# Optimization experiments

Measured on AMD Instinct MI355X. Metric: run time of the kernel, lower is better.

Reference implementation:

```python
import jax, jax.numpy as jnp
import numpy as np

D_MODEL = 1024
D_STATE = 16
D_CONV = 4
EXPAND = 1
D_INNER = EXPAND * D_MODEL  # must equal D_MODEL for original dt_proj shapes to work
BATCH = 2
SEQ = 2048


def silu(x):
    return x * jax.nn.sigmoid(x)


def setup_inputs() -> dict:
    key = jax.random.key(0)
    ks = jax.random.split(key, 8)
    s = 0.02
    return {
        "x": jax.random.normal(ks[0], (BATCH, SEQ, D_MODEL), dtype=jnp.float32),
        "W_in": jax.random.normal(ks[1], (2 * D_INNER, D_MODEL), dtype=jnp.float32) * s,
        "conv_w": jax.random.normal(ks[2], (D_INNER, D_CONV), dtype=jnp.float32) * s,
        "conv_b": jnp.zeros((D_INNER,), dtype=jnp.float32),
        "W_dt": jax.random.normal(ks[3], (D_INNER, D_INNER), dtype=jnp.float32) * s,
        "b_dt": jnp.zeros((D_INNER,), dtype=jnp.float32),
        "A_log": jnp.zeros((D_INNER, D_STATE), dtype=jnp.float32),  # torch: log(ones)=0
        "Bp": jax.random.normal(ks[4], (D_INNER, D_STATE), dtype=jnp.float32),
        "Cp": jax.random.normal(ks[5], (D_INNER, D_STATE), dtype=jnp.float32),
        "Dp": jnp.ones((D_INNER,), dtype=jnp.float32),
        "W_out": jax.random.normal(ks[6], (D_MODEL, D_INNER), dtype=jnp.float32) * s,
    }


def reference(x, W_in, conv_w, conv_b, W_dt, b_dt, A_log, Bp, Cp, Dp, W_out):
    B, L, _ = x.shape
    # in_proj then split into ssm branch and gating residual
    xr = x @ W_in.T                               # (B, L, 2*D_INNER)
    x_proj, res = jnp.split(xr, 2, axis=-1)       # each (B, L, D_INNER)

    # causal depthwise conv1d (kernel D_CONV), == torch conv1d(padding=K-1)[..., :L]
    xp = jnp.pad(x_proj, ((0, 0), (D_CONV - 1, 0), (0, 0)))
    xc = conv_b + sum(conv_w[:, k] * xp[:, k:k + L, :] for k in range(D_CONV))
    xc = silu(xc)                                 # (B, L, D_INNER)

    # selective SSM scan
    delta = jax.nn.softplus(xc @ W_dt.T + b_dt)   # (B, L, D_INNER)
    A = -jnp.exp(A_log)                           # (D_INNER, D_STATE)
    dA = jnp.exp(delta[..., None] * A)            # (B, L, D_INNER, D_STATE)
    dBx = delta[..., None] * Bp * xc[..., None]   # (B, L, D_INNER, D_STATE)

    def step(h, inp):
        dA_t, dBx_t = inp                         # (B, D_INNER, D_STATE)
        h = dA_t * h + dBx_t
        y = jnp.einsum('bdn,dn->bd', h, Cp)
        return h, y

    h0 = jnp.zeros((B, D_INNER, D_STATE), dtype=x.dtype)
    _, ys = jax.lax.scan(step, h0, (dA.transpose(1, 0, 2, 3), dBx.transpose(1, 0, 2, 3)))
    x_ssm = ys.transpose(1, 0, 2) + xc * Dp       # (B, L, D_INNER)

    return (x_ssm * silu(res)) @ W_out.T          # (B, L, D_MODEL)
```

## Files before the change

### kernel.cpp

```cpp
#include <hip/hip_runtime.h>

typedef unsigned short u16;
typedef __bf16 bf16;
typedef bf16 bf16x8 __attribute__((ext_vector_type(8)));
typedef float f32x16 __attribute__((ext_vector_type(16)));

#define SEQ     2048
#define BATCH   2
#define DM      1024
#define DI      1024
#define NROW    (BATCH*SEQ)
#define NSTATE  16
#define NCHUNK  64
#define CLEN    32
#define BK      64

static_assert(SEQ == NCHUNK * CLEN, "chunking must cover SEQ");

__device__ __forceinline__ u16 f2bf(float f) {
  unsigned u = __builtin_bit_cast(unsigned, f);
  u += 0x7FFFu + ((u >> 16) & 1u);
  return (u16)(u >> 16);
}
__device__ __forceinline__ float bf2f(u16 u) {
  return __builtin_bit_cast(float, (unsigned)u << 16);
}
__device__ __forceinline__ float sigm(float x) { return 1.f / (1.f + __expf(-x)); }

__global__ __launch_bounds__(256) void k_cvt_all(
    const float* __restrict__ x, const float* __restrict__ Win,
    const float* __restrict__ Wdt, const float* __restrict__ Wout,
    u16* __restrict__ xbf, u16* __restrict__ winbf,
    u16* __restrict__ wdtbf, u16* __restrict__ woutbf)
{
  long i = (long)blockIdx.x * 256 + threadIdx.x;
  const float* src; u16* dst; long off;
  if (i < 1048576)            { src = x;    dst = xbf;    off = i; }
  else if (i < 1572864)       { src = Win;  dst = winbf;  off = i - 1048576; }
  else if (i < 1835008)       { src = Wdt;  dst = wdtbf;  off = i - 1572864; }
  else                        { src = Wout; dst = woutbf; off = i - 1835008; }
  float4 v = reinterpret_cast<const float4*>(src)[off];
  ushort4 o;
  o.x = f2bf(v.x); o.y = f2bf(v.y); o.z = f2bf(v.z); o.w = f2bf(v.w);
  reinterpret_cast<ushort4*>(dst)[off] = o;
}


__device__ __forceinline__ void gload16(const u16* g, u16* l) {
  __builtin_amdgcn_global_load_lds((const __attribute__((address_space(1))) void*)g,
                                   (__attribute__((address_space(3))) void*)l,
                                   16, 0, 0);
}

template<int EPI, int BM, int BN, int GX, int MINW>
__global__ __launch_bounds__(256, MINW) void k_gemm(
    const u16* __restrict__ A, const u16* __restrict__ B,
    float* __restrict__ outf, u16* __restrict__ outb, u16* __restrict__ outb2,
    const float* __restrict__ bias,
    const float* __restrict__ A_log, const float* __restrict__ Bp,
    float* __restrict__ hfin, float* __restrict__ sumdt,
    int M, int N, int K)
{
  constexpr int MI_ = BM / 64;
  constexpr int NI_ = BN / 64;
  __shared__ __align__(16) u16 sA[2 * BM * BK];
  __shared__ __align__(16) u16 sB[2 * BN * BK];
  const int t = threadIdx.x;
  const int wave = t >> 6, lane = t & 63;
  const int la = lane & 31, hi = lane >> 5;
  const int wr = wave >> 1, wc = wave & 1;

  const int nwg = gridDim.x;
  const int bid = blockIdx.x;
  const int wg  = (bid & 7) * (nwg >> 3) + (bid >> 3);
  const long bm = (long)(wg / GX) * BM;
  const long bn = (long)(wg % GX) * BN;

  f32x16 acc[MI_][NI_] = {};

  const int srow = t >> 3;
  const int gslot8 = (((t & 7) ^ (srow & 7)) * 8);
  const u16* gA0 = A + (bm + srow) * (long)K + gslot8;
  const u16* gB0 = B + (bn + srow) * (long)K + gslot8;

  auto STAGE = [&](int buf, int k0) {
    #pragma unroll
    for (int i = 0; i < BM / 32; ++i)
      gload16(gA0 + (long)i * 32 * K + k0,
              &sA[buf * (BM * BK) + i * 2048 + wave * 512]);
    #pragma unroll
    for (int i = 0; i < BN / 32; ++i)
      gload16(gB0 + (long)i * 32 * K + k0,
              &sB[buf * (BN * BK) + i * 2048 + wave * 512]);
  };

  const int xr = la & 7;
  STAGE(0, 0);
  __syncthreads();
  int cur = 0;
  for (int k0 = 0; k0 < K; k0 += BK) {
    if (k0 + BK < K) STAGE(cur ^ 1, k0 + BK);
    const u16* pa = &sA[cur * (BM * BK)];
    const u16* pb = &sB[cur * (BN * BK)];
    bf16x8 af[4][MI_], bfr[4][NI_];
    #pragma unroll
    for (int ks = 0; ks < 4; ++ks) {
      const int co = ((ks * 2 + hi) ^ xr) * 8;
      #pragma unroll
      for (int mi = 0; mi < MI_; ++mi)
        af[ks][mi] = *reinterpret_cast<const bf16x8*>(
            pa + (wr * (BM / 2) + mi * 32 + la) * BK + co);
      #pragma unroll
      for (int ni = 0; ni < NI_; ++ni)
        bfr[ks][ni] = *reinterpret_cast<const bf16x8*>(
            pb + (wc * (BN / 2) + ni * 32 + la) * BK + co);
    }
    __builtin_amdgcn_s_setprio(1);
    #pragma unroll
    for (int ks = 0; ks < 4; ++ks)
      #pragma unroll
      for (int mi = 0; mi < MI_; ++mi)
        #pragma unroll
        for (int ni = 0; ni < NI_; ++ni)
          acc[mi][ni] = __builtin_amdgcn_mfma_f32_32x32x16_bf16(
              af[ks][mi], bfr[ks][ni], acc[mi][ni], 0, 0, 0);
    __builtin_amdgcn_s_setprio(0);
    __syncthreads();
    cur ^= 1;
  }

  float* sDelta = (float*)sA;

  #pragma unroll
  for (int mi = 0; mi < MI_; ++mi) {
    const long rowb = bm + wr * (BM / 2) + mi * 32 + 4 * hi;
    #pragma unroll
    for (int ni = 0; ni < NI_; ++ni) {
      const long col = bn + wc * (BN / 2) + ni * 32 + la;
      #pragma unroll
      for (int q = 0; q < 4; ++q)
        #pragma unroll
        for (int j = 0; j < 4; ++j) {
          const float v = acc[mi][ni][q * 4 + j];
          const long r = rowb + q * 8 + j;
          if (EPI == 0) {
            outf[r * N + col] = v;
          } else if (EPI == 1) {
            if (bn < DI) outb[r * DI + col] = f2bf(v);
            else         outb2[r * DI + (col - DI)] = f2bf(v * sigm(v));
          } else if (EPI == 3) {
            float z = v + bias[col];
            float sp = fmaxf(z, 0.f) + log1pf(__expf(-fabsf(z)));
            outb[r * N + col] = f2bf(sp);
            sDelta[(int)(r - bm) * 64 + (int)(col - bn)] = sp;
          }
        }
    }
  }

  if (EPI == 3) {
    __syncthreads();
    const int pair = t >> 1, half = t & 1;
    const int clocal = pair >> 6;
    const int dl = pair & 63;
    const int d = (int)bn + dl;
    const int b = (int)(bm >> 11);
    const int cglob = (int)((bm & 2047) >> 5) + clocal;
    const long grow0 = bm + clocal * 32;
    float Aa[8], Bb[8], h[8];
    #pragma unroll
    for (int n = 0; n < 8; ++n) {
      Aa[n] = -__expf(A_log[d * NSTATE + half * 8 + n]);
      Bb[n] = Bp[d * NSTATE + half * 8 + n];
      h[n] = 0.f;
    }
    float sdt = 0.f;
    for (int i = 0; i < CLEN; ++i) {
      float dt = sDelta[(clocal * 32 + i) * 64 + dl];
      float xv = bf2f(A[(grow0 + i) * (long)K + d]);
      sdt += dt;
      float dx = dt * xv;
      #pragma unroll
      for (int n = 0; n < 8; ++n) {
        float da = __expf(dt * Aa[n]);
        h[n] = fmaf(da, h[n], dx * Bb[n]);
      }
    }
    const long hb = ((long)(b * NCHUNK + cglob) * NSTATE + half * 8) * DI + d;
    #pragma unroll
    for (int n = 0; n < 8; ++n) hfin[hb + (long)n * DI] = h[n];
    if (half == 0) sumdt[(long)(b * NCHUNK + cglob) * DI + d] = sdt;
  }
}

__global__ __launch_bounds__(256) void k_conv(
    const u16* __restrict__ xproj, const float* __restrict__ convw,
    const float* __restrict__ convb, u16* __restrict__ xcbf)
{
  const int idx = blockIdx.x * 256 + threadIdx.x;
  const int d0 = (idx & 127) * 8;
  const int m  = idx >> 7;
  const int l  = m & (SEQ - 1);
  float acc[8];
  #pragma unroll
  for (int di = 0; di < 8; ++di) acc[di] = convb[d0 + di];
  #pragma unroll
  for (int k = 0; k < 4; ++k) {
    if (l + k - 3 >= 0) {
      ushort4 v2 = *reinterpret_cast<const ushort4*>(&xproj[(long)(m + k - 3) * DI + d0]);
      ushort4 v3 = *reinterpret_cast<const ushort4*>(&xproj[(long)(m + k - 3) * DI + d0 + 4]);
      const u16 vv[8] = {v2.x, v2.y, v2.z, v2.w, v3.x, v3.y, v3.z, v3.w};
      #pragma unroll
      for (int di = 0; di < 8; ++di)
        acc[di] = fmaf(convw[(d0 + di) * 4 + k], bf2f(vv[di]), acc[di]);
    }
  }
  ushort4 o0, o1;
  u16 ov[8];
  #pragma unroll
  for (int di = 0; di < 8; ++di) {
    float s = acc[di] * sigm(acc[di]);
    ov[di] = f2bf(s);
  }
  o0 = {ov[0], ov[1], ov[2], ov[3]}; o1 = {ov[4], ov[5], ov[6], ov[7]};
  *reinterpret_cast<ushort4*>(&xcbf[(long)m * DI + d0]) = o0;
  *reinterpret_cast<ushort4*>(&xcbf[(long)m * DI + d0 + 4]) = o1;
}

__global__ __launch_bounds__(256) void k_combine(
    const float* __restrict__ hfin, const float* __restrict__ sumdt_buf,
    const float* __restrict__ A_log, float* __restrict__ hstart)
{
  const int idx = blockIdx.x * 256 + threadIdx.x;
  const int d = idx & (DI - 1);
  const int n = (idx >> 10) & (NSTATE - 1);
  const int b = idx >> 14;
  const float Aa = -__expf(A_log[d * NSTATE + n]);
  float h = 0.f;
  for (int c = 0; c < NCHUNK; ++c) {
    const long sb = ((long)(b * NCHUNK + c) * NSTATE + n) * DI + d;
    hstart[sb] = h;
    float sdt = sumdt_buf[(long)(b * NCHUNK + c) * DI + d];
    h = fmaf(__expf(Aa * sdt), h, hfin[sb]);
  }
}

__global__ __launch_bounds__(256) void k_scanB(
    const u16* __restrict__ delta, const u16* __restrict__ xc,
    const float* __restrict__ A_log, const float* __restrict__ Bp,
    const float* __restrict__ Cp, const float* __restrict__ Dp,
    const u16* __restrict__ sres, const float* __restrict__ hstart,
    u16* __restrict__ gated)
{
  const int tid = threadIdx.x, blk = blockIdx.x;
  const int d = (blk & 3) * 256 + tid;
  const int c = (blk >> 2) & (NCHUNK - 1);
  const int b = blk >> 8;
  float Aa[NSTATE], Bb[NSTATE], Cc[NSTATE], h[NSTATE];
  #pragma unroll
  for (int n = 0; n < NSTATE; ++n) {
    Aa[n] = -__expf(A_log[d * NSTATE + n]);
    Bb[n] = Bp[d * NSTATE + n];
    Cc[n] = Cp[d * NSTATE + n];
  }
  const float Dd = Dp[d];
  const long sb = ((long)(b * NCHUNK + c) * NSTATE) * DI + d;
  #pragma unroll
  for (int n = 0; n < NSTATE; ++n) h[n] = hstart[sb + (long)n * DI];
  const long base = ((long)(b * SEQ + c * CLEN)) * DI + d;
  for (int i = 0; i < CLEN; ++i) {
    float dt = bf2f(delta[base + (long)i * DI]);
    float x  = bf2f(xc[base + (long)i * DI]);
    float dx = dt * x;
    float y = 0.f;
    #pragma unroll
    for (int n = 0; n < NSTATE; ++n) {
      float da = __expf(dt * Aa[n]);
      h[n] = fmaf(da, h[n], dx * Bb[n]);
      y = fmaf(h[n], Cc[n], y);
    }
    float xs = fmaf(x, Dd, y);
    float g = xs * bf2f(sres[base + (long)i * DI]);
    gated[base + (long)i * DI] = f2bf(g);
  }
}

extern "C" void kernel_launch(void* const* d_in, const int* in_sizes, int n_in,
                              void* d_out, int out_size, void* d_ws, size_t ws_size,
                              hipStream_t stream)
{
  const float* x      = (const float*)d_in[0];
  const float* W_in   = (const float*)d_in[1];
  const float* conv_w = (const float*)d_in[2];
  const float* conv_b = (const float*)d_in[3];
  const float* W_dt   = (const float*)d_in[4];
  const float* b_dt   = (const float*)d_in[5];
  const float* A_log  = (const float*)d_in[6];
  const float* Bp     = (const float*)d_in[7];
  const float* Cp     = (const float*)d_in[8];
  const float* Dp     = (const float*)d_in[9];
  const float* W_out  = (const float*)d_in[10];
  float* out = (float*)d_out;

  const long MD = (long)NROW * DI;

  char* ws = (char*)d_ws;
  u16*   xproj_bf = (u16*)ws;               ws += MD * 2;
  u16*   silu_bf  = (u16*)ws;               ws += MD * 2;
  u16*   delta_bf = (u16*)ws;               ws += MD * 2;
  u16*   xc_bf    = (u16*)ws;               ws += MD * 2;
  u16*   xbf      = (u16*)ws;               ws += MD * 2;
  u16*   Win_bf   = (u16*)ws;               ws += (long)2 * DI * DM * 2;
  u16*   Wdt_bf   = (u16*)ws;               ws += (long)DI * DI * 2;
  u16*   Wout_bf  = (u16*)ws;               ws += (long)DM * DI * 2;
  float* hfin     = (float*)ws;             ws += (long)BATCH * NCHUNK * NSTATE * DI * 4;
  float* sumdt    = (float*)ws;             ws += (long)BATCH * NCHUNK * DI * 4;
  float* hstart   = (float*)ws;             ws += (long)BATCH * NCHUNK * NSTATE * DI * 4;

  u16* gated = xbf;

  k_cvt_all<<<dim3(8192), dim3(256), 0, stream>>>(
      x, W_in, W_dt, W_out, xbf, Win_bf, Wdt_bf, Wout_bf);

  k_gemm<1, 128, 128, 16, 2><<<dim3(512), dim3(256), 0, stream>>>(
      xbf, Win_bf, nullptr, xproj_bf, silu_bf, nullptr,
      nullptr, nullptr, nullptr, nullptr, NROW, 2 * DI, DM);

  k_conv<<<dim3((unsigned)(MD / 8 / 256)), dim3(256), 0, stream>>>(
      xproj_bf, conv_w, conv_b, xc_bf);

  k_gemm<3, 64, 64, 16, 2><<<dim3(1024), dim3(256), 0, stream>>>(
      xc_bf, Wdt_bf, nullptr, delta_bf, nullptr, b_dt,
      A_log, Bp, hfin, sumdt, NROW, DI, DI);

  k_combine<<<dim3(BATCH * NSTATE * DI / 256), dim3(256), 0, stream>>>(
      hfin, sumdt, A_log, hstart);
  k_scanB<<<dim3(BATCH * NCHUNK * (DI / 256)), dim3(256), 0, stream>>>(
      delta_bf, xc_bf, A_log, Bp, Cp, Dp, silu_bf, hstart, gated);

  k_gemm<0, 64, 64, 16, 4><<<dim3(1024), dim3(256), 0, stream>>>(
      gated, Wout_bf, out, nullptr, nullptr, nullptr,
      nullptr, nullptr, nullptr, nullptr, NROW, DM, DI);
}
```

Baseline: 165.9 us.

## Unify GEMMs on 128x128 tiles with 16x16x32 MFMA and rebalance scan epilogue

Every GEMM now uses one 128x128 tile shape computed with 16x16x32 bf16 MFMAs instead of 32x32x16. The delta and out-projection GEMMs move from 1024 blocks of 64x64 to 256 blocks of 128x128. The aim is more operand reuse per LDS load and fewer redundant global reads. The fused chunk-scan epilogue is reorganised so each thread handles all 16 states for two chunks serially, which gives fewer parallel threads and longer serial dependency chains on a grid of only 256 blocks.

```diff
diff --git a/kernel.cpp b/kernel.cpp
--- a/kernel.cpp
+++ b/kernel.cpp
@@ -3,7 +3,7 @@
 typedef unsigned short u16;
 typedef __bf16 bf16;
 typedef bf16 bf16x8 __attribute__((ext_vector_type(8)));
-typedef float f32x16 __attribute__((ext_vector_type(16)));
+typedef float f32x4 __attribute__((ext_vector_type(4)));
 
 #define SEQ     2048
 #define BATCH   2
@@ -13,7 +13,6 @@
 #define NSTATE  16
 #define NCHUNK  64
 #define CLEN    32
-#define BK      64
 
 static_assert(SEQ == NCHUNK * CLEN, "chunking must cover SEQ");
 
@@ -52,8 +51,8 @@
                                    16, 0, 0);
 }
 
-template<int EPI, int BM, int BN, int GX, int MINW>
-__global__ __launch_bounds__(256, MINW) void k_gemm(
+template<int EPI, int GX>
+__global__ __launch_bounds__(256, 2) void k_gemm(
     const u16* __restrict__ A, const u16* __restrict__ B,
     float* __restrict__ outf, u16* __restrict__ outb, u16* __restrict__ outb2,
     const float* __restrict__ bias,
@@ -61,22 +60,20 @@
     float* __restrict__ hfin, float* __restrict__ sumdt,
     int M, int N, int K)
 {
-  constexpr int MI_ = BM / 64;
-  constexpr int NI_ = BN / 64;
-  __shared__ __align__(16) u16 sA[2 * BM * BK];
-  __shared__ __align__(16) u16 sB[2 * BN * BK];
+  __shared__ __align__(16) u16 smem[4 * 128 * 64];
+  u16* sA = smem;
+  u16* sB = smem + 2 * 128 * 64;
   const int t = threadIdx.x;
   const int wave = t >> 6, lane = t & 63;
-  const int la = lane & 31, hi = lane >> 5;
+  const int lr = lane & 15, kb = lane >> 4;
   const int wr = wave >> 1, wc = wave & 1;
 
-  const int nwg = gridDim.x;
-  const int bid = blockIdx.x;
+  const int nwg = gridDim.x, bid = blockIdx.x;
   const int wg  = (bid & 7) * (nwg >> 3) + (bid >> 3);
-  const long bm = (long)(wg / GX) * BM;
-  const long bn = (long)(wg % GX) * BN;
-
-  f32x16 acc[MI_][NI_] = {};
+  const long bm = (long)(wg / GX) * 128;
+  const long bn = (long)(wg % GX) * 128;
+
+  f32x4 acc[4][4] = {};
 
   const int srow = t >> 3;
   const int gslot8 = (((t & 7) ^ (srow & 7)) * 8);
@@ -85,111 +82,110 @@
 
   auto STAGE = [&](int buf, int k0) {
     #pragma unroll
-    for (int i = 0; i < BM / 32; ++i)
-      gload16(gA0 + (long)i * 32 * K + k0,
-              &sA[buf * (BM * BK) + i * 2048 + wave * 512]);
-    #pragma unroll
-    for (int i = 0; i < BN / 32; ++i)
-      gload16(gB0 + (long)i * 32 * K + k0,
-              &sB[buf * (BN * BK) + i * 2048 + wave * 512]);
+    for (int i = 0; i < 4; ++i)
+      gload16(gA0 + (long)i * 32 * K + k0, &sA[buf * 8192 + i * 2048 + wave * 512]);
+    #pragma unroll
+    for (int i = 0; i < 4; ++i)
+      gload16(gB0 + (long)i * 32 * K + k0, &sB[buf * 8192 + i * 2048 + wave * 512]);
   };
 
-  const int xr = la & 7;
+  const int xr = lr & 7;
   STAGE(0, 0);
   __syncthreads();
   int cur = 0;
-  for (int k0 = 0; k0 < K; k0 += BK) {
-    if (k0 + BK < K) STAGE(cur ^ 1, k0 + BK);
-    const u16* pa = &sA[cur * (BM * BK)];
-    const u16* pb = &sB[cur * (BN * BK)];
-    bf16x8 af[4][MI_], bfr[4][NI_];
-    #pragma unroll
-    for (int ks = 0; ks < 4; ++ks) {
-      const int co = ((ks * 2 + hi) ^ xr) * 8;
-      #pragma unroll
-      for (int mi = 0; mi < MI_; ++mi)
+  for (int k0 = 0; k0 < K; k0 += 64) {
+    if (k0 + 64 < K) STAGE(cur ^ 1, k0 + 64);
+    const u16* pa = &sA[cur * 8192];
+    const u16* pb = &sB[cur * 8192];
+    bf16x8 af[2][4], bfr[2][4];
+    #pragma unroll
+    for (int ks = 0; ks < 2; ++ks) {
+      const int co = ((ks * 4 + kb) ^ xr) * 8;
+      #pragma unroll
+      for (int mi = 0; mi < 4; ++mi)
         af[ks][mi] = *reinterpret_cast<const bf16x8*>(
-            pa + (wr * (BM / 2) + mi * 32 + la) * BK + co);
-      #pragma unroll
-      for (int ni = 0; ni < NI_; ++ni)
+            pa + (wr * 64 + mi * 16 + lr) * 64 + co);
+      #pragma unroll
+      for (int ni = 0; ni < 4; ++ni)
         bfr[ks][ni] = *reinterpret_cast<const bf16x8*>(
-            pb + (wc * (BN / 2) + ni * 32 + la) * BK + co);
+            pb + (wc * 64 + ni * 16 + lr) * 64 + co);
     }
     __builtin_amdgcn_s_setprio(1);
     #pragma unroll
-    for (int ks = 0; ks < 4; ++ks)
-      #pragma unroll
-      for (int mi = 0; mi < MI_; ++mi)
+    for (int ks = 0; ks < 2; ++ks)
+      #pragma unroll
+      for (int mi = 0; mi < 4; ++mi)
         #pragma unroll
-        for (int ni = 0; ni < NI_; ++ni)
-          acc[mi][ni] = __builtin_amdgcn_mfma_f32_32x32x16_bf16(
+        for (int ni = 0; ni < 4; ++ni)
+          acc[mi][ni] = __builtin_amdgcn_mfma_f32_16x16x32_bf16(
               af[ks][mi], bfr[ks][ni], acc[mi][ni], 0, 0, 0);
     __builtin_amdgcn_s_setprio(0);
     __syncthreads();
     cur ^= 1;
   }
 
-  float* sDelta = (float*)sA;
-
-  #pragma unroll
-  for (int mi = 0; mi < MI_; ++mi) {
-    const long rowb = bm + wr * (BM / 2) + mi * 32 + 4 * hi;
-    #pragma unroll
-    for (int ni = 0; ni < NI_; ++ni) {
-      const long col = bn + wc * (BN / 2) + ni * 32 + la;
-      #pragma unroll
-      for (int q = 0; q < 4; ++q)
-        #pragma unroll
-        for (int j = 0; j < 4; ++j) {
-          const float v = acc[mi][ni][q * 4 + j];
-          const long r = rowb + q * 8 + j;
-          if (EPI == 0) {
-            outf[r * N + col] = v;
-          } else if (EPI == 1) {
-            if (bn < DI) outb[r * DI + col] = f2bf(v);
-            else         outb2[r * DI + (col - DI)] = f2bf(v * sigm(v));
-          } else if (EPI == 3) {
-            float z = v + bias[col];
-            float sp = fmaxf(z, 0.f) + log1pf(__expf(-fabsf(z)));
-            outb[r * N + col] = f2bf(sp);
-            sDelta[(int)(r - bm) * 64 + (int)(col - bn)] = sp;
-          }
+  float* sDelta = (float*)smem;
+
+  #pragma unroll
+  for (int mi = 0; mi < 4; ++mi) {
+    const long row0 = bm + wr * 64 + mi * 16 + kb * 4;
+    #pragma unroll
+    for (int ni = 0; ni < 4; ++ni) {
+      const long col = bn + wc * 64 + ni * 16 + lr;
+      #pragma unroll
+      for (int j = 0; j < 4; ++j) {
+        const float v = acc[mi][ni][j];
+        const long r = row0 + j;
+        if (EPI == 0) {
+          outf[r * N + col] = v;
+        } else if (EPI == 1) {
+          if (bn < DI) outb[r * DI + col] = f2bf(v);
+          else         outb2[r * DI + (col - DI)] = f2bf(v * sigm(v));
+        } else if (EPI == 3) {
+          float z = v + bias[col];
+          float sp = fmaxf(z, 0.f) + log1pf(__expf(-fabsf(z)));
+          outb[r * N + col] = f2bf(sp);
+          sDelta[(int)(r - bm) * 128 + (int)(col - bn)] = sp;
         }
+      }
     }
   }
 
   if (EPI == 3) {
     __syncthreads();
-    const int pair = t >> 1, half = t & 1;
-    const int clocal = pair >> 6;
-    const int dl = pair & 63;
-    const int d = (int)bn + dl;
-    const int b = (int)(bm >> 11);
-    const int cglob = (int)((bm & 2047) >> 5) + clocal;
-    const long grow0 = bm + clocal * 32;
-    float Aa[8], Bb[8], h[8];
-    #pragma unroll
-    for (int n = 0; n < 8; ++n) {
-      Aa[n] = -__expf(A_log[d * NSTATE + half * 8 + n]);
-      Bb[n] = Bp[d * NSTATE + half * 8 + n];
-      h[n] = 0.f;
-    }
-    float sdt = 0.f;
-    for (int i = 0; i < CLEN; ++i) {
-      float dt = sDelta[(clocal * 32 + i) * 64 + dl];
-      float xv = bf2f(A[(grow0 + i) * (long)K + d]);
-      sdt += dt;
-      float dx = dt * xv;
-      #pragma unroll
-      for (int n = 0; n < 8; ++n) {
-        float da = __expf(dt * Aa[n]);
-        h[n] = fmaf(da, h[n], dx * Bb[n]);
+    const int dl = t & 127;
+    const int d  = (int)bn + dl;
+    const int b  = (int)(bm >> 11);
+    const int c0 = (int)((bm & 2047) >> 5);
+    float Aa[NSTATE], Bb[NSTATE];
+    #pragma unroll
+    for (int n = 0; n < NSTATE; ++n) {
+      Aa[n] = -__expf(A_log[d * NSTATE + n]);
+      Bb[n] = Bp[d * NSTATE + n];
+    }
+    for (int cl = (t >> 7) * 2; cl < (t >> 7) * 2 + 2; ++cl) {
+      float h[NSTATE];
+      #pragma unroll
+      for (int n = 0; n < NSTATE; ++n) h[n] = 0.f;
+      float sdt = 0.f;
+      const long grow0 = bm + cl * 32;
+      for (int i = 0; i < CLEN; ++i) {
+        float dt = sDelta[(cl * 32 + i) * 128 + dl];
+        float xv = bf2f(A[(grow0 + i) * (long)K + d]);
+        sdt += dt;
+        float dx = dt * xv;
+        #pragma unroll
+        for (int n = 0; n < NSTATE; ++n) {
+          float da = __expf(dt * Aa[n]);
+          h[n] = fmaf(da, h[n], dx * Bb[n]);
+        }
       }
-    }
-    const long hb = ((long)(b * NCHUNK + cglob) * NSTATE + half * 8) * DI + d;
-    #pragma unroll
-    for (int n = 0; n < 8; ++n) hfin[hb + (long)n * DI] = h[n];
-    if (half == 0) sumdt[(long)(b * NCHUNK + cglob) * DI + d] = sdt;
+      const int cg = c0 + cl;
+      const long hb = ((long)(b * NCHUNK + cg) * NSTATE) * DI + d;
+      #pragma unroll
+      for (int n = 0; n < NSTATE; ++n) hfin[hb + (long)n * DI] = h[n];
+      sumdt[(long)(b * NCHUNK + cg) * DI + d] = sdt;
+    }
   }
 }
 
@@ -215,14 +211,13 @@
         acc[di] = fmaf(convw[(d0 + di) * 4 + k], bf2f(vv[di]), acc[di]);
     }
   }
-  ushort4 o0, o1;
   u16 ov[8];
   #pragma unroll
   for (int di = 0; di < 8; ++di) {
     float s = acc[di] * sigm(acc[di]);
     ov[di] = f2bf(s);
   }
-  o0 = {ov[0], ov[1], ov[2], ov[3]}; o1 = {ov[4], ov[5], ov[6], ov[7]};
+  ushort4 o0 = {ov[0], ov[1], ov[2], ov[3]}, o1 = {ov[4], ov[5], ov[6], ov[7]};
   *reinterpret_cast<ushort4*>(&xcbf[(long)m * DI + d0]) = o0;
   *reinterpret_cast<ushort4*>(&xcbf[(long)m * DI + d0 + 4]) = o1;
 }
@@ -322,14 +317,14 @@
   k_cvt_all<<<dim3(8192), dim3(256), 0, stream>>>(
       x, W_in, W_dt, W_out, xbf, Win_bf, Wdt_bf, Wout_bf);
 
-  k_gemm<1, 128, 128, 16, 2><<<dim3(512), dim3(256), 0, stream>>>(
+  k_gemm<1, 16><<<dim3(512), dim3(256), 0, stream>>>(
       xbf, Win_bf, nullptr, xproj_bf, silu_bf, nullptr,
       nullptr, nullptr, nullptr, nullptr, NROW, 2 * DI, DM);
 
   k_conv<<<dim3((unsigned)(MD / 8 / 256)), dim3(256), 0, stream>>>(
       xproj_bf, conv_w, conv_b, xc_bf);
 
-  k_gemm<3, 64, 64, 16, 2><<<dim3(1024), dim3(256), 0, stream>>>(
+  k_gemm<3, 8><<<dim3(256), dim3(256), 0, stream>>>(
       xc_bf, Wdt_bf, nullptr, delta_bf, nullptr, b_dt,
       A_log, Bp, hfin, sumdt, NROW, DI, DI);
 
@@ -338,7 +333,7 @@
   k_scanB<<<dim3(BATCH * NCHUNK * (DI / 256)), dim3(256), 0, stream>>>(
       delta_bf, xc_bf, A_log, Bp, Cp, Dp, silu_bf, hstart, gated);
 
-  k_gemm<0, 64, 64, 16, 4><<<dim3(1024), dim3(256), 0, stream>>>(
+  k_gemm<0, 8><<<dim3(256), dim3(256), 0, stream>>>(
       gated, Wout_bf, out, nullptr, nullptr, nullptr,
       nullptr, nullptr, nullptr, nullptr, NROW, DM, DI);
 }
```

Result: slower. 169.5 us (+2.2%).

## Use 128x64 tiles for dt and out GEMMs, one thread per channel chunk scan

Applied to the files above, without the earlier changes.

Enlarges the M tile of the dt_proj and out_proj GEMMs from 64 to 128 rows, halving the grid to 512 workgroups to improve operand reuse. The fused chunk-scan epilogue is restructured so each thread handles all 16 states of one channel over a 32-step chunk, which fits the new 128-row tile (4 chunks x 64 channels). It also drops the s_setprio hints and fixes launch bounds at 2 waves per SIMD for all GEMMs. The risks are fewer workgroups for the 256 CUs, higher register pressure from 16-state arrays, and a serial scan per thread that is twice as long.

```diff
diff --git a/kernel.cpp b/kernel.cpp
--- a/kernel.cpp
+++ b/kernel.cpp
@@ -52,8 +52,8 @@
                                    16, 0, 0);
 }
 
-template<int EPI, int BM, int BN, int GX, int MINW>
-__global__ __launch_bounds__(256, MINW) void k_gemm(
+template<int EPI, int BM, int BN, int GX>
+__global__ __launch_bounds__(256, 2) void k_gemm(
     const u16* __restrict__ A, const u16* __restrict__ B,
     float* __restrict__ outf, u16* __restrict__ outb, u16* __restrict__ outb2,
     const float* __restrict__ bias,
@@ -70,8 +70,7 @@
   const int la = lane & 31, hi = lane >> 5;
   const int wr = wave >> 1, wc = wave & 1;
 
-  const int nwg = gridDim.x;
-  const int bid = blockIdx.x;
+  const int nwg = gridDim.x, bid = blockIdx.x;
   const int wg  = (bid & 7) * (nwg >> 3) + (bid >> 3);
   const long bm = (long)(wg / GX) * BM;
   const long bn = (long)(wg % GX) * BN;
@@ -115,7 +114,6 @@
         bfr[ks][ni] = *reinterpret_cast<const bf16x8*>(
             pb + (wc * (BN / 2) + ni * 32 + la) * BK + co);
     }
-    __builtin_amdgcn_s_setprio(1);
     #pragma unroll
     for (int ks = 0; ks < 4; ++ks)
       #pragma unroll
@@ -124,7 +122,6 @@
         for (int ni = 0; ni < NI_; ++ni)
           acc[mi][ni] = __builtin_amdgcn_mfma_f32_32x32x16_bf16(
               af[ks][mi], bfr[ks][ni], acc[mi][ni], 0, 0, 0);
-    __builtin_amdgcn_s_setprio(0);
     __syncthreads();
     cur ^= 1;
   }
@@ -152,7 +149,7 @@
             float z = v + bias[col];
             float sp = fmaxf(z, 0.f) + log1pf(__expf(-fabsf(z)));
             outb[r * N + col] = f2bf(sp);
-            sDelta[(int)(r - bm) * 64 + (int)(col - bn)] = sp;
+            sDelta[(int)(r - bm) * BN + (int)(col - bn)] = sp;
           }
         }
     }
@@ -160,36 +157,35 @@
 
   if (EPI == 3) {
     __syncthreads();
-    const int pair = t >> 1, half = t & 1;
-    const int clocal = pair >> 6;
-    const int dl = pair & 63;
-    const int d = (int)bn + dl;
-    const int b = (int)(bm >> 11);
-    const int cglob = (int)((bm & 2047) >> 5) + clocal;
-    const long grow0 = bm + clocal * 32;
-    float Aa[8], Bb[8], h[8];
-    #pragma unroll
-    for (int n = 0; n < 8; ++n) {
-      Aa[n] = -__expf(A_log[d * NSTATE + half * 8 + n]);
-      Bb[n] = Bp[d * NSTATE + half * 8 + n];
+    const int cl = t >> 6;
+    const int dl = t & 63;
+    const int d  = (int)bn + dl;
+    const int b  = (int)(bm >> 11);
+    const int cg = (int)((bm & 2047) >> 5) + cl;
+    float Aa[NSTATE], Bb[NSTATE], h[NSTATE];
+    #pragma unroll
+    for (int n = 0; n < NSTATE; ++n) {
+      Aa[n] = -__expf(A_log[d * NSTATE + n]);
+      Bb[n] = Bp[d * NSTATE + n];
       h[n] = 0.f;
     }
     float sdt = 0.f;
+    const long grow0 = bm + cl * 32;
     for (int i = 0; i < CLEN; ++i) {
-      float dt = sDelta[(clocal * 32 + i) * 64 + dl];
+      float dt = sDelta[(cl * 32 + i) * BN + dl];
       float xv = bf2f(A[(grow0 + i) * (long)K + d]);
       sdt += dt;
       float dx = dt * xv;
       #pragma unroll
-      for (int n = 0; n < 8; ++n) {
+      for (int n = 0; n < NSTATE; ++n) {
         float da = __expf(dt * Aa[n]);
         h[n] = fmaf(da, h[n], dx * Bb[n]);
       }
     }
-    const long hb = ((long)(b * NCHUNK + cglob) * NSTATE + half * 8) * DI + d;
-    #pragma unroll
-    for (int n = 0; n < 8; ++n) hfin[hb + (long)n * DI] = h[n];
-    if (half == 0) sumdt[(long)(b * NCHUNK + cglob) * DI + d] = sdt;
+    const long hb = ((long)(b * NCHUNK + cg) * NSTATE) * DI + d;
+    #pragma unroll
+    for (int n = 0; n < NSTATE; ++n) hfin[hb + (long)n * DI] = h[n];
+    sumdt[(long)(b * NCHUNK + cg) * DI + d] = sdt;
   }
 }
 
@@ -215,14 +211,13 @@
         acc[di] = fmaf(convw[(d0 + di) * 4 + k], bf2f(vv[di]), acc[di]);
     }
   }
-  ushort4 o0, o1;
   u16 ov[8];
   #pragma unroll
   for (int di = 0; di < 8; ++di) {
     float s = acc[di] * sigm(acc[di]);
     ov[di] = f2bf(s);
   }
-  o0 = {ov[0], ov[1], ov[2], ov[3]}; o1 = {ov[4], ov[5], ov[6], ov[7]};
+  ushort4 o0 = {ov[0], ov[1], ov[2], ov[3]}, o1 = {ov[4], ov[5], ov[6], ov[7]};
   *reinterpret_cast<ushort4*>(&xcbf[(long)m * DI + d0]) = o0;
   *reinterpret_cast<ushort4*>(&xcbf[(long)m * DI + d0 + 4]) = o1;
 }
@@ -322,14 +317,14 @@
   k_cvt_all<<<dim3(8192), dim3(256), 0, stream>>>(
       x, W_in, W_dt, W_out, xbf, Win_bf, Wdt_bf, Wout_bf);
 
-  k_gemm<1, 128, 128, 16, 2><<<dim3(512), dim3(256), 0, stream>>>(
+  k_gemm<1, 128, 128, 16><<<dim3(512), dim3(256), 0, stream>>>(
       xbf, Win_bf, nullptr, xproj_bf, silu_bf, nullptr,
       nullptr, nullptr, nullptr, nullptr, NROW, 2 * DI, DM);
 
   k_conv<<<dim3((unsigned)(MD / 8 / 256)), dim3(256), 0, stream>>>(
       xproj_bf, conv_w, conv_b, xc_bf);
 
-  k_gemm<3, 64, 64, 16, 2><<<dim3(1024), dim3(256), 0, stream>>>(
+  k_gemm<3, 128, 64, 16><<<dim3(512), dim3(256), 0, stream>>>(
       xc_bf, Wdt_bf, nullptr, delta_bf, nullptr, b_dt,
       A_log, Bp, hfin, sumdt, NROW, DI, DI);
 
@@ -338,7 +333,7 @@
   k_scanB<<<dim3(BATCH * NCHUNK * (DI / 256)), dim3(256), 0, stream>>>(
       delta_bf, xc_bf, A_log, Bp, Cp, Dp, silu_bf, hstart, gated);
 
-  k_gemm<0, 64, 64, 16, 4><<<dim3(1024), dim3(256), 0, stream>>>(
+  k_gemm<0, 128, 64, 16><<<dim3(512), dim3(256), 0, stream>>>(
       gated, Wout_bf, out, nullptr, nullptr, nullptr,
       nullptr, nullptr, nullptr, nullptr, NROW, DM, DI);
 }
```

After: 166.4 us. About the same (+0.3%).
